# Kernel tuning notes

Measured on AMD Instinct MI355X. Metric: run time of the kernel, lower is better.

## Reference

```python
import jax, jax.numpy as jnp
import numpy as np

NUM_GROUPS = 16
EPS = 1e-6


def setup_inputs() -> dict:
    key = jax.random.key(0)
    k1, k2, k3, k4 = jax.random.split(key, 4)
    B, N = 16, 131072
    pred = jax.random.normal(k1, (B, N, 3), dtype=jnp.float32)
    target = jax.random.normal(k2, (B, N, 3), dtype=jnp.float32)
    mask = jax.random.randint(k3, (B, N), 0, 2, dtype=jnp.int32)
    groups = jax.random.randint(k4, (B, N), 0, NUM_GROUPS, dtype=jnp.int32)
    return {"pred": pred, "target": target, "mask": mask, "groups": groups}


def _group_median_normalizer(z, valid, groups):
    """Per-point depth normalizer: lower-median of |z| within each (batch, group)
    over valid points, clamped to EPS; groups with no valid points get 1.0.
    z, valid, groups: (B, N). Returns (B, N)."""
    gids = jnp.arange(NUM_GROUPS, dtype=groups.dtype)
    in_g = (groups[:, None, :] == gids[None, :, None]) & valid[:, None, :]  # (B,G,N)
    inf = jnp.asarray(jnp.inf, z.dtype)
    z_g = jnp.where(in_g, z[:, None, :], inf)        # (B,G,N), invalid -> +inf
    z_sorted = jnp.sort(z_g, axis=-1)                # valid values occupy first cnt slots
    cnt = jnp.sum(in_g, axis=-1)                     # (B,G)
    idx = jnp.maximum(cnt - 1, 0) // 2               # torch lower median index
    med = jnp.take_along_axis(z_sorted, idx[..., None], axis=-1)[..., 0]  # (B,G)
    # empty groups give +inf -> nan_to_num -> 1.0, matching torch's untouched default
    med = jnp.nan_to_num(med, nan=1.0, posinf=1.0, neginf=1.0)
    med_safe = jnp.maximum(jnp.abs(med), EPS)        # clamp(|median|, min=eps)
    return jnp.take_along_axis(med_safe, groups, axis=-1)  # gather per point (B,N)


def _log_transform(x):
    return jnp.sign(x) * jnp.log1p(jnp.abs(x))


def reference(pred, target, mask, groups):
    valid = mask.astype(bool)                        # (B,N)
    # shared depth normalization: denominator from TARGET, used for both
    norm = _group_median_normalizer(target[..., 2], valid, groups)  # (B,N)
    vm = valid[..., None]                            # (B,N,1)
    inv = 1.0 / norm[..., None]
    p = jnp.nan_to_num(jnp.where(vm, pred, 0.0) * inv, nan=0.0, posinf=0.0, neginf=0.0)
    t = jnp.nan_to_num(jnp.where(vm, target, 0.0) * inv, nan=0.0, posinf=0.0, neginf=0.0)
    loss = jnp.abs(_log_transform(p) - _log_transform(t))  # (B,N,3)
    loss = jnp.where(vm, loss, 0.0)
    denom = 3.0 * jnp.sum(valid).astype(jnp.float32) + 1e-6  # expanded mask count
    return jnp.sum(loss) / denom
```

## Files before the change

### kernel.cpp

```cpp
#include <hip/hip_runtime.h>
#include <math.h>

#define NPTS_N 131072
#define NGROUP 16
#define NBG 256
#define CBLK 512
#define BPB 32
#define PPB 4096
#define SEGCAP 256
#define NSEL 6144
#define NACC 64
#define LGRID 1024
#define EPSF 1e-6f

__device__ __forceinline__ unsigned f2key(float f) {
    unsigned u = __float_as_uint(f);
    return (u & 0x80000000u) ? ~u : (u | 0x80000000u);
}
__device__ __forceinline__ float key2f(unsigned k) {
    unsigned u = (k & 0x80000000u) ? (k ^ 0x80000000u) : ~k;
    return __uint_as_float(u);
}
__device__ __forceinline__ float flog1p(float a) {
    return __log2f(1.0f + a) * 0.69314718056f;
}

__global__ __launch_bounds__(256) void compact_kernel(
        const float* __restrict__ target,
        const int* __restrict__ mask,
        const int* __restrict__ groups,
        unsigned* __restrict__ bucket,
        unsigned* __restrict__ blockCnt,
        unsigned char* __restrict__ packed) {
    __shared__ unsigned scnt[NGROUP];
    int tid = threadIdx.x, blk = blockIdx.x;
    int i0 = blk * PPB + tid * 16;
    if (tid < NGROUP) scnt[tid] = 0;
    __syncthreads();
    int4 m[4], g[4];
    #pragma unroll
    for (int k = 0; k < 4; ++k) {
        m[k] = *(const int4*)(mask + i0 + k * 4);
        g[k] = *(const int4*)(groups + i0 + k * 4);
    }
    unsigned pk[4];
    unsigned keys[16]; unsigned meta[16]; unsigned vbits = 0;
    #pragma unroll
    for (int k = 0; k < 4; ++k) {
        int mm[4] = {m[k].x, m[k].y, m[k].z, m[k].w};
        int gg[4] = {g[k].x, g[k].y, g[k].z, g[k].w};
        unsigned pb = 0;
        #pragma unroll
        for (int j = 0; j < 4; ++j) {
            int idx = k * 4 + j;
            unsigned gj = (unsigned)gg[j] & 15u;
            pb |= (gj | (mm[j] ? 0x80u : 0u)) << (8 * j);
            if (mm[j]) {
                keys[idx] = f2key(target[(size_t)(i0 + idx) * 3 + 2]);
                unsigned pos = atomicAdd(&scnt[gj], 1u);
                meta[idx] = (gj << 16) | pos;
                vbits |= 1u << idx;
            }
        }
        pk[k] = pb;
    }
    *(uint4*)(packed + i0) = make_uint4(pk[0], pk[1], pk[2], pk[3]);
    __syncthreads();
    if (tid < NGROUP) blockCnt[blk * NGROUP + tid] = scnt[tid];
    #pragma unroll
    for (int idx = 0; idx < 16; ++idx) {
        if (vbits & (1u << idx)) {
            unsigned gj = meta[idx] >> 16, pos = meta[idx] & 0xFFFFu;
            if (pos < SEGCAP)
                bucket[(size_t)(blk * NGROUP + gj) * SEGCAP + pos] = keys[idx];
        }
    }
}

__global__ __launch_bounds__(256) void select_kernel(
        const unsigned* __restrict__ bucket,
        const unsigned* __restrict__ blockCnt,
        float* __restrict__ norm,
        unsigned* __restrict__ cnt,
        float* __restrict__ accF,
        unsigned* __restrict__ done) {
    __shared__ unsigned skey[NSEL];
    __shared__ unsigned hist[2048];
    __shared__ unsigned sc[BPB];
    __shared__ unsigned segoff[BPB + 1];
    __shared__ unsigned wsum[4];
    __shared__ unsigned sres[2];
    int bg = blockIdx.x, tid = threadIdx.x;
    int b = bg >> 4, g = bg & 15;
    if (bg == 0) {
        if (tid < NACC) accF[tid] = 0.f;
        if (tid == NACC) *done = 0;
    }
    if (tid < BPB) {
        unsigned s = blockCnt[(b * BPB + tid) * NGROUP + g];
        sc[tid] = s;
        unsigned inc = s;
        #pragma unroll
        for (int o = 1; o < BPB; o <<= 1) {
            unsigned v = __shfl_up(inc, o, 64);
            if (tid >= o) inc += v;
        }
        segoff[tid + 1] = inc;
        if (tid == 0) segoff[0] = 0;
    }
    __syncthreads();
    unsigned ntrue = segoff[BPB];
    unsigned n = ntrue > NSEL ? NSEL : ntrue;
    if (tid == 0) cnt[bg] = ntrue;
    if (n == 0) { if (tid == 0) norm[bg] = 1.0f; return; }
    int wv = tid >> 6, ln = tid & 63;
    for (int c = wv; c < BPB; c += 4) {
        unsigned count = sc[c], o = segoff[c];
        if (count > SEGCAP) count = SEGCAP;
        const unsigned* src = bucket + (size_t)((b * BPB + c) * NGROUP + g) * SEGCAP;
        for (unsigned j = ln; j < count; j += 64)
            if (o + j < NSEL) skey[o + j] = src[j];
    }
    __syncthreads();

    unsigned rank = (n - 1) >> 1;
    unsigned selkey = 0;
    const int shifts[3] = {21, 10, 0};
    const int widths[3] = {11, 11, 10};
    for (int p = 0; p < 3; ++p) {
        int sft = shifts[p], w = widths[p];
        unsigned nb = 1u << w, bmask = nb - 1;
        for (unsigned j = tid; j < nb; j += 256) hist[j] = 0;
        __syncthreads();
        for (unsigned j = tid; j < n; j += 256) {
            unsigned key = skey[j];
            bool in = (p == 0) || ((key >> (sft + w)) == selkey);
            if (in) atomicAdd(&hist[(key >> sft) & bmask], 1u);
        }
        __syncthreads();
        unsigned cpl = nb >> 8;
        unsigned basebin = tid * cpl;
        unsigned s = 0;
        for (unsigned j = 0; j < cpl; ++j) s += hist[basebin + j];
        unsigned inc = s;
        #pragma unroll
        for (int o = 1; o < 64; o <<= 1) {
            unsigned v = __shfl_up(inc, o, 64);
            if ((tid & 63) >= o) inc += v;
        }
        if ((tid & 63) == 63) wsum[tid >> 6] = inc;
        __syncthreads();
        unsigned woff = 0;
        for (int w2 = 0; w2 < (tid >> 6); ++w2) woff += wsum[w2];
        unsigned excl = woff + inc - s;
        if (rank >= excl && rank < excl + s) {
            unsigned run = excl, binSel = basebin;
            for (unsigned j = 0; j < cpl; ++j) {
                unsigned h = hist[basebin + j];
                if (run + h > rank) { binSel = basebin + j; break; }
                run += h;
            }
            sres[0] = binSel; sres[1] = rank - run;
        }
        __syncthreads();
        selkey = (selkey << w) | sres[0];
        rank = sres[1];
        __syncthreads();
    }
    if (tid == 0) norm[bg] = fmaxf(fabsf(key2f(selkey)), EPSF);
}

__global__ __launch_bounds__(256) void loss_kernel(
        const float* __restrict__ pred,
        const float* __restrict__ target,
        const unsigned char* __restrict__ packed,
        const float* __restrict__ norm,
        const unsigned* __restrict__ cnt,
        float* __restrict__ accF,
        unsigned* __restrict__ done,
        float* __restrict__ out) {
    __shared__ float sinv[NGROUP];
    __shared__ float swsum[4];
    __shared__ bool isLast;
    __shared__ float red[256];
    __shared__ float accSum;
    int tid = threadIdx.x;
    int blk = blockIdx.x;
    int b = blk >> 6;
    if (tid < NGROUP) sinv[tid] = 1.0f / norm[(b << 4) + tid];
    __syncthreads();
    int p0 = b * NPTS_N + (blk & 63) * 2048 + tid * 8;
    uint2 pkw = *(const uint2*)(packed + p0);
    const float4* pr4 = (const float4*)(pred + (size_t)p0 * 3);
    const float4* tg4 = (const float4*)(target + (size_t)p0 * 3);
    float pv[24], tv[24];
    #pragma unroll
    for (int k = 0; k < 6; ++k) { *(float4*)(pv + 4 * k) = pr4[k]; *(float4*)(tv + 4 * k) = tg4[k]; }
    float acc = 0.f;
    #pragma unroll
    for (int q = 0; q < 8; ++q) {
        unsigned byte = ((q < 4 ? pkw.x : pkw.y) >> (8 * (q & 3))) & 0xFFu;
        if (byte & 0x80u) {
            float inv = sinv[byte & 15u];
            #pragma unroll
            for (int c = 0; c < 3; ++c) {
                float pp = pv[q * 3 + c] * inv;
                float tt = tv[q * 3 + c] * inv;
                float lp = copysignf(flog1p(fabsf(pp)), pp);
                float lt = copysignf(flog1p(fabsf(tt)), tt);
                acc += fabsf(lp - lt);
            }
        }
    }
    #pragma unroll
    for (int off = 32; off; off >>= 1) acc += __shfl_down(acc, off, 64);
    if ((tid & 63) == 0) swsum[tid >> 6] = acc;
    __syncthreads();
    if (tid == 0) {
        float v = swsum[0] + swsum[1] + swsum[2] + swsum[3];
        atomicAdd(&accF[blk & (NACC - 1)], v);
        __asm__ volatile("s_waitcnt vmcnt(0)" ::: "memory");
        unsigned old = __hip_atomic_fetch_add(done, 1u, __ATOMIC_RELAXED,
                                              __HIP_MEMORY_SCOPE_AGENT);
        isLast = (old == (unsigned)(LGRID - 1));
    }
    __syncthreads();
    if (isLast) {
        float s = 0.f;
        if (tid < NACC)
            s = __hip_atomic_load(&accF[tid], __ATOMIC_RELAXED, __HIP_MEMORY_SCOPE_AGENT);
        #pragma unroll
        for (int off = 32; off; off >>= 1) s += __shfl_down(s, off, 64);
        if (tid == 0) accSum = s;
        red[tid] = (float)cnt[tid];
        __syncthreads();
        for (int st = 128; st; st >>= 1) {
            if (tid < st) red[tid] += red[tid + st];
            __syncthreads();
        }
        if (tid == 0) out[0] = accSum / (3.0f * red[0] + 1e-6f);
    }
}

extern "C" void kernel_launch(void* const* d_in, const int* in_sizes, int n_in,
                              void* d_out, int out_size, void* d_ws, size_t ws_size,
                              hipStream_t stream) {
    const float* pred   = (const float*)d_in[0];
    const float* target = (const float*)d_in[1];
    const int*   mask   = (const int*)d_in[2];
    const int*   groups = (const int*)d_in[3];
    float* out = (float*)d_out;

    char* ws = (char*)d_ws;
    const size_t MB = 1024 * 1024;
    unsigned*      bucket   = (unsigned*)ws;
    unsigned char* packed   = (unsigned char*)(ws + 8 * MB);
    unsigned*      blockCnt = (unsigned*)(ws + 10 * MB);
    unsigned*      cnt      = (unsigned*)(ws + 10 * MB + 32768);
    float*         normv    = (float*)(ws + 10 * MB + 32768 + 1024);
    float*         accF     = (float*)(ws + 10 * MB + 32768 + 2048);
    unsigned*      done     = (unsigned*)(ws + 10 * MB + 32768 + 3072);

    compact_kernel<<<dim3(CBLK), dim3(256), 0, stream>>>(target, mask, groups,
                                                         bucket, blockCnt, packed);
    select_kernel<<<dim3(NBG), dim3(256), 0, stream>>>(bucket, blockCnt, normv, cnt, accF, done);
    loss_kernel<<<dim3(LGRID), dim3(256), 0, stream>>>(pred, target, packed, normv,
                                                       cnt, accF, done, out);
}
```

Measured before the change: 134.0 us.

## Fuse compaction and median select via global histogram and last-block selection

Merges the compaction and selection kernels into one. Each block builds a global 4096-bin histogram of the high key bits per (batch, group) with atomics and appends keys to per-group arrays via global atomic offsets. The last block per batch then finds the median bin from the histogram and picks the exact median by rank-counting the few candidate keys in shared memory. This replaces the three-pass in-block radix select and the segment gather with one pass plus a small candidate sort, at the cost of a zeroing kernel, heavy global atomic contention, and capacity caps (GCAP, MCAP) that drop keys if a group or median bin overflows.

```diff
diff --git a/kernel.cpp b/kernel.cpp
--- a/kernel.cpp
+++ b/kernel.cpp
@@ -4,11 +4,13 @@
 #define NPTS_N 131072
 #define NGROUP 16
 #define NBG 256
-#define CBLK 512
-#define BPB 32
-#define PPB 4096
-#define SEGCAP 256
-#define NSEL 6144
+#define CBLK 256
+#define TPB 1024
+#define BPB 16
+#define PPB 8192
+#define GCAP 6144
+#define HBINS 4096
+#define MCAP 768
 #define NACC 64
 #define LGRID 1024
 #define EPSF 1e-6f
@@ -25,149 +27,142 @@
     return __log2f(1.0f + a) * 0.69314718056f;
 }
 
-__global__ __launch_bounds__(256) void compact_kernel(
+__global__ __launch_bounds__(256) void zero_kernel(uint4* p, int n4) {
+    int i = blockIdx.x * blockDim.x + threadIdx.x;
+    int stride = gridDim.x * blockDim.x;
+    for (; i < n4; i += stride) p[i] = make_uint4(0u, 0u, 0u, 0u);
+}
+
+__global__ __launch_bounds__(1024) void compsel_kernel(
         const float* __restrict__ target,
         const int* __restrict__ mask,
         const int* __restrict__ groups,
-        unsigned* __restrict__ bucket,
-        unsigned* __restrict__ blockCnt,
-        unsigned char* __restrict__ packed) {
+        unsigned* __restrict__ gkeys,
+        unsigned char* __restrict__ packed,
+        unsigned* __restrict__ hist,
+        unsigned* __restrict__ gbase,
+        unsigned* __restrict__ batchDone,
+        float* __restrict__ normv) {
     __shared__ unsigned scnt[NGROUP];
-    int tid = threadIdx.x, blk = blockIdx.x;
-    int i0 = blk * PPB + tid * 16;
+    __shared__ unsigned sbase[NGROUP];
+    __shared__ unsigned mcnt[NGROUP];
+    __shared__ unsigned mkeys[NGROUP][MCAP];
+    __shared__ bool sLast;
+    const int tid = threadIdx.x, blk = blockIdx.x;
+    const int b = blk >> 4;
+    const int i0 = blk * PPB + tid * 8;
     if (tid < NGROUP) scnt[tid] = 0;
     __syncthreads();
-    int4 m[4], g[4];
-    #pragma unroll
-    for (int k = 0; k < 4; ++k) {
+    int4 m[2], g[2];
+    #pragma unroll
+    for (int k = 0; k < 2; ++k) {
         m[k] = *(const int4*)(mask + i0 + k * 4);
         g[k] = *(const int4*)(groups + i0 + k * 4);
     }
-    unsigned pk[4];
-    unsigned keys[16]; unsigned meta[16]; unsigned vbits = 0;
-    #pragma unroll
-    for (int k = 0; k < 4; ++k) {
+    float f[24];
+    const float4* t4 = (const float4*)(target + (size_t)i0 * 3);
+    #pragma unroll
+    for (int k = 0; k < 6; ++k) *(float4*)(f + 4 * k) = t4[k];
+    unsigned pkw[2] = {0u, 0u};
+    unsigned keys[8], meta[8], vbits = 0;
+    #pragma unroll
+    for (int k = 0; k < 2; ++k) {
         int mm[4] = {m[k].x, m[k].y, m[k].z, m[k].w};
         int gg[4] = {g[k].x, g[k].y, g[k].z, g[k].w};
-        unsigned pb = 0;
         #pragma unroll
         for (int j = 0; j < 4; ++j) {
             int idx = k * 4 + j;
             unsigned gj = (unsigned)gg[j] & 15u;
-            pb |= (gj | (mm[j] ? 0x80u : 0u)) << (8 * j);
+            pkw[k] |= (gj | (mm[j] ? 0x80u : 0u)) << (8 * j);
             if (mm[j]) {
-                keys[idx] = f2key(target[(size_t)(i0 + idx) * 3 + 2]);
+                unsigned key = f2key(f[3 * idx + 2]);
+                keys[idx] = key;
                 unsigned pos = atomicAdd(&scnt[gj], 1u);
                 meta[idx] = (gj << 16) | pos;
                 vbits |= 1u << idx;
+                atomicAdd(&hist[(size_t)(b * NGROUP + gj) * HBINS + (key >> 20)], 1u);
             }
         }
-        pk[k] = pb;
-    }
-    *(uint4*)(packed + i0) = make_uint4(pk[0], pk[1], pk[2], pk[3]);
-    __syncthreads();
-    if (tid < NGROUP) blockCnt[blk * NGROUP + tid] = scnt[tid];
-    #pragma unroll
-    for (int idx = 0; idx < 16; ++idx) {
+    }
+    *(uint2*)(packed + i0) = make_uint2(pkw[0], pkw[1]);
+    __syncthreads();
+    if (tid < NGROUP)
+        sbase[tid] = atomicAdd(&gbase[b * NGROUP + tid], scnt[tid]);
+    __syncthreads();
+    #pragma unroll
+    for (int idx = 0; idx < 8; ++idx) {
         if (vbits & (1u << idx)) {
-            unsigned gj = meta[idx] >> 16, pos = meta[idx] & 0xFFFFu;
-            if (pos < SEGCAP)
-                bucket[(size_t)(blk * NGROUP + gj) * SEGCAP + pos] = keys[idx];
-        }
-    }
-}
-
-__global__ __launch_bounds__(256) void select_kernel(
-        const unsigned* __restrict__ bucket,
-        const unsigned* __restrict__ blockCnt,
-        float* __restrict__ norm,
-        unsigned* __restrict__ cnt,
-        float* __restrict__ accF,
-        unsigned* __restrict__ done) {
-    __shared__ unsigned skey[NSEL];
-    __shared__ unsigned hist[2048];
-    __shared__ unsigned sc[BPB];
-    __shared__ unsigned segoff[BPB + 1];
-    __shared__ unsigned wsum[4];
-    __shared__ unsigned sres[2];
-    int bg = blockIdx.x, tid = threadIdx.x;
-    int b = bg >> 4, g = bg & 15;
-    if (bg == 0) {
-        if (tid < NACC) accF[tid] = 0.f;
-        if (tid == NACC) *done = 0;
-    }
-    if (tid < BPB) {
-        unsigned s = blockCnt[(b * BPB + tid) * NGROUP + g];
-        sc[tid] = s;
-        unsigned inc = s;
-        #pragma unroll
-        for (int o = 1; o < BPB; o <<= 1) {
-            unsigned v = __shfl_up(inc, o, 64);
-            if (tid >= o) inc += v;
-        }
-        segoff[tid + 1] = inc;
-        if (tid == 0) segoff[0] = 0;
-    }
-    __syncthreads();
-    unsigned ntrue = segoff[BPB];
-    unsigned n = ntrue > NSEL ? NSEL : ntrue;
-    if (tid == 0) cnt[bg] = ntrue;
-    if (n == 0) { if (tid == 0) norm[bg] = 1.0f; return; }
-    int wv = tid >> 6, ln = tid & 63;
-    for (int c = wv; c < BPB; c += 4) {
-        unsigned count = sc[c], o = segoff[c];
-        if (count > SEGCAP) count = SEGCAP;
-        const unsigned* src = bucket + (size_t)((b * BPB + c) * NGROUP + g) * SEGCAP;
-        for (unsigned j = ln; j < count; j += 64)
-            if (o + j < NSEL) skey[o + j] = src[j];
-    }
-    __syncthreads();
-
+            unsigned gj = meta[idx] >> 16;
+            unsigned pos = (meta[idx] & 0xFFFFu) + sbase[gj];
+            if (pos < GCAP)
+                gkeys[(size_t)(b * NGROUP + gj) * GCAP + pos] = keys[idx];
+        }
+    }
+    __syncthreads();
+    if (tid == 0) {
+        unsigned old = __hip_atomic_fetch_add(&batchDone[b], 1u, __ATOMIC_RELEASE,
+                                              __HIP_MEMORY_SCOPE_AGENT);
+        sLast = (old == (unsigned)(BPB - 1));
+    }
+    __syncthreads();
+    if (!sLast) return;
+    __threadfence();
+
+    const int wv = tid >> 6, ln = tid & 63;
+    const int bg = b * NGROUP + wv;
+    unsigned n = __hip_atomic_load(&gbase[bg], __ATOMIC_RELAXED,
+                                   __HIP_MEMORY_SCOPE_AGENT);
+    if (n == 0) { if (ln == 0) normv[bg] = 1.0f; return; }
     unsigned rank = (n - 1) >> 1;
-    unsigned selkey = 0;
-    const int shifts[3] = {21, 10, 0};
-    const int widths[3] = {11, 11, 10};
-    for (int p = 0; p < 3; ++p) {
-        int sft = shifts[p], w = widths[p];
-        unsigned nb = 1u << w, bmask = nb - 1;
-        for (unsigned j = tid; j < nb; j += 256) hist[j] = 0;
-        __syncthreads();
-        for (unsigned j = tid; j < n; j += 256) {
-            unsigned key = skey[j];
-            bool in = (p == 0) || ((key >> (sft + w)) == selkey);
-            if (in) atomicAdd(&hist[(key >> sft) & bmask], 1u);
-        }
-        __syncthreads();
-        unsigned cpl = nb >> 8;
-        unsigned basebin = tid * cpl;
-        unsigned s = 0;
-        for (unsigned j = 0; j < cpl; ++j) s += hist[basebin + j];
-        unsigned inc = s;
-        #pragma unroll
-        for (int o = 1; o < 64; o <<= 1) {
-            unsigned v = __shfl_up(inc, o, 64);
-            if ((tid & 63) >= o) inc += v;
-        }
-        if ((tid & 63) == 63) wsum[tid >> 6] = inc;
-        __syncthreads();
-        unsigned woff = 0;
-        for (int w2 = 0; w2 < (tid >> 6); ++w2) woff += wsum[w2];
-        unsigned excl = woff + inc - s;
-        if (rank >= excl && rank < excl + s) {
-            unsigned run = excl, binSel = basebin;
-            for (unsigned j = 0; j < cpl; ++j) {
-                unsigned h = hist[basebin + j];
-                if (run + h > rank) { binSel = basebin + j; break; }
-                run += h;
-            }
-            sres[0] = binSel; sres[1] = rank - run;
-        }
-        __syncthreads();
-        selkey = (selkey << w) | sres[0];
-        rank = sres[1];
-        __syncthreads();
-    }
-    if (tid == 0) norm[bg] = fmaxf(fabsf(key2f(selkey)), EPSF);
+    const unsigned* hb = hist + (size_t)bg * HBINS;
+    unsigned lsum = 0;
+    for (int k = 0; k < 16; ++k) {
+        uint4 h = *(const uint4*)(hb + ln * 64 + k * 4);
+        lsum += h.x + h.y + h.z + h.w;
+    }
+    unsigned inc = lsum;
+    #pragma unroll
+    for (int o = 1; o < 64; o <<= 1) {
+        unsigned v = __shfl_up(inc, o, 64);
+        if (ln >= o) inc += v;
+    }
+    unsigned excl = inc - lsum;
+    bool has = (rank >= excl) && (rank < excl + lsum);
+    unsigned binB = 0, rr = 0;
+    if (has) {
+        unsigned run = excl;
+        for (int j = 0; j < 64; ++j) {
+            unsigned h = hb[ln * 64 + j];
+            if (run + h > rank) { binB = (unsigned)(ln * 64 + j); rr = rank - run; break; }
+            run += h;
+        }
+    }
+    unsigned long long bal = __ballot(has);
+    int src = __ffsll(bal) - 1;
+    binB = __shfl(binB, src, 64);
+    rr = __shfl(rr, src, 64);
+    if (ln == 0) mcnt[wv] = 0;
+    unsigned nc = n > GCAP ? GCAP : n;
+    const unsigned* kp = gkeys + (size_t)bg * GCAP;
+    for (unsigned j = ln; j < nc; j += 64) {
+        unsigned key = kp[j];
+        if ((key >> 20) == binB) {
+            unsigned p = atomicAdd(&mcnt[wv], 1u);
+            if (p < MCAP) mkeys[wv][p] = key;
+        }
+    }
+    unsigned m2 = mcnt[wv]; if (m2 > MCAP) m2 = MCAP;
+    for (unsigned j = ln; j < m2; j += 64) {
+        unsigned kj = mkeys[wv][j];
+        unsigned cl = 0, ce = 0;
+        for (unsigned i = 0; i < m2; ++i) {
+            unsigned ki = mkeys[wv][i];
+            cl += (ki < kj) ? 1u : 0u;
+            ce += (ki == kj) ? 1u : 0u;
+        }
+        if (cl <= rr && rr < cl + ce)
+            normv[bg] = fmaxf(fabsf(key2f(kj)), EPSF);
+    }
 }
 
 __global__ __launch_bounds__(256) void loss_kernel(
@@ -175,7 +170,7 @@
         const float* __restrict__ target,
         const unsigned char* __restrict__ packed,
         const float* __restrict__ norm,
-        const unsigned* __restrict__ cnt,
+        const unsigned* __restrict__ gbase,
         float* __restrict__ accF,
         unsigned* __restrict__ done,
         float* __restrict__ out) {
@@ -232,7 +227,7 @@
         #pragma unroll
         for (int off = 32; off; off >>= 1) s += __shfl_down(s, off, 64);
         if (tid == 0) accSum = s;
-        red[tid] = (float)cnt[tid];
+        red[tid] = (float)gbase[tid];
         __syncthreads();
         for (int st = 128; st; st >>= 1) {
             if (tid < st) red[tid] += red[tid + st];
@@ -253,17 +248,21 @@
 
     char* ws = (char*)d_ws;
     const size_t MB = 1024 * 1024;
-    unsigned*      bucket   = (unsigned*)ws;
-    unsigned char* packed   = (unsigned char*)(ws + 8 * MB);
-    unsigned*      blockCnt = (unsigned*)(ws + 10 * MB);
-    unsigned*      cnt      = (unsigned*)(ws + 10 * MB + 32768);
-    float*         normv    = (float*)(ws + 10 * MB + 32768 + 1024);
-    float*         accF     = (float*)(ws + 10 * MB + 32768 + 2048);
-    unsigned*      done     = (unsigned*)(ws + 10 * MB + 32768 + 3072);
-
-    compact_kernel<<<dim3(CBLK), dim3(256), 0, stream>>>(target, mask, groups,
-                                                         bucket, blockCnt, packed);
-    select_kernel<<<dim3(NBG), dim3(256), 0, stream>>>(bucket, blockCnt, normv, cnt, accF, done);
+    unsigned*      gkeys   = (unsigned*)ws;
+    unsigned char* packed  = (unsigned char*)(ws + 6 * MB);
+    float*         normv   = (float*)(ws + 8 * MB);
+    char*          zbase   = ws + 8 * MB + 4096;
+    unsigned*      hist    = (unsigned*)zbase;
+    unsigned*      gbase   = (unsigned*)(zbase + 4 * MB);
+    unsigned*      batchDone = (unsigned*)(zbase + 4 * MB + 1024);
+    float*         accF    = (float*)(zbase + 4 * MB + 1088);
+    unsigned*      done    = (unsigned*)(zbase + 4 * MB + 1344);
+    const int      n4      = (int)((4 * MB + 4096) / 16);
+
+    zero_kernel<<<dim3(512), dim3(256), 0, stream>>>((uint4*)zbase, n4);
+    compsel_kernel<<<dim3(CBLK), dim3(TPB), 0, stream>>>(target, mask, groups,
+                                                         gkeys, packed, hist,
+                                                         gbase, batchDone, normv);
     loss_kernel<<<dim3(LGRID), dim3(256), 0, stream>>>(pred, target, packed, normv,
-                                                       cnt, accF, done, out);
-}
+                                                       gbase, accF, done, out);
+}
```

Result: slower. 209.5 us (+56.3%).
